# Kernel optimization log

Measured on AMD Instinct MI355X. Metric: run time of the kernel, lower is better.

Reference implementation:

```python
import jax, jax.numpy as jnp
import numpy as np

E = 1024
H = 16
D = E // H  # head_dim = 64


def setup_inputs() -> dict:
    key = jax.random.key(0)
    k_x, k_w1, k_b1, k_w2, k_b2 = jax.random.split(key, 5)
    s = 1.0 / np.sqrt(E)
    return {
        "x": jax.random.normal(k_x, (2, 2048, E), dtype=jnp.float32),
        "qkv_w": jax.random.uniform(k_w1, (3 * E, E), jnp.float32, -s, s),
        "qkv_b": jax.random.uniform(k_b1, (3 * E,), jnp.float32, -s, s),
        "out_w": jax.random.uniform(k_w2, (E, E), jnp.float32, -s, s),
        "out_b": jax.random.uniform(k_b2, (E,), jnp.float32, -s, s),
    }


def reference(x, qkv_w, qkv_b, out_w, out_b):
    B, T, _ = x.shape
    # qkv projection (torch Linear: x @ W.T + b)
    qkv = x @ qkv_w.T + qkv_b  # [B, T, 3E]
    q, k, v = jnp.split(qkv, 3, axis=-1)
    # [B, T, E] -> [B, H, T, D]
    def to_heads(t):
        return t.reshape(B, T, H, D).transpose(0, 2, 1, 3)
    q, k, v = to_heads(q), to_heads(k), to_heads(v)
    scale = 1.0 / np.sqrt(D).astype(np.float32)
    scores = jnp.einsum("bhqd,bhkd->bhqk", q, k) * scale  # [B, H, T, T]
    attn = jax.nn.softmax(scores, axis=-1)
    # dropout is identity in eval mode
    out = jnp.einsum("bhqk,bhkd->bhqd", attn, v)  # [B, H, T, D]
    out = out.transpose(0, 2, 1, 3).reshape(B, T, E)
    return out @ out_w.T + out_b
```

## Files before the change

kernel.cpp:

```cpp
#include <hip/hip_runtime.h>

#define TT 2048
#define BB 2
#define EE 1024
#define HH 16
#define DD 64
#define E3 3072
#define NTOK 4096

typedef unsigned short u16;
typedef _Float16 __attribute__((ext_vector_type(8))) half8;
typedef __fp16 __attribute__((ext_vector_type(2))) fp16x2;
typedef __attribute__((ext_vector_type(4))) float f32x4;

__device__ __forceinline__ unsigned f2h(float f) {
    union { _Float16 h; u16 u; } v; v.h = (_Float16)f; return (unsigned)v.u;
}
__device__ __forceinline__ unsigned pkh(float a, float b) {
    union { fp16x2 h; unsigned u; } v;
    v.h = __builtin_amdgcn_cvt_pkrtz(a, b);
    return v.u;
}

__device__ __forceinline__ void async_ld16(const u16* g, const u16* l) {
    auto gp = reinterpret_cast<const __attribute__((address_space(1))) unsigned*>(
        reinterpret_cast<uintptr_t>(g));
    auto lp = reinterpret_cast<__attribute__((address_space(3))) unsigned*>(
        reinterpret_cast<uintptr_t>(l));
    __builtin_amdgcn_global_load_lds(gp, lp, 16, 0, 0);
}

__global__ __launch_bounds__(256) void split3(
    const float* __restrict__ x, const float* __restrict__ w1,
    const float* __restrict__ w2,
    u16* __restrict__ xh, u16* __restrict__ w1h, u16* __restrict__ w2h)
{
    const int N1 = (NTOK * EE) / 4;
    const int N2 = N1 + (E3 * EE) / 4;
    int i = blockIdx.x * 256 + threadIdx.x;
    const float* src; u16* dst; int j;
    if (i < N1)      { src = x;  dst = xh;  j = i; }
    else if (i < N2) { src = w1; dst = w1h; j = i - N1; }
    else             { src = w2; dst = w2h; j = i - N2; }
    float4 v = ((const float4*)src)[j];
    *(uint2*)&dst[(size_t)j * 4] = make_uint2(
        f2h(v.x) | (f2h(v.y) << 16), f2h(v.z) | (f2h(v.w) << 16));
}

__global__ __launch_bounds__(256) void vtrans(
    const u16* __restrict__ qkv, u16* __restrict__ vt)
{
    __shared__ u16 L[64][72];
    const int tid = threadIdx.x;
    const int t0 = blockIdx.x * 64;
    const int h  = blockIdx.y;
    const int b  = blockIdx.z;
    const int row = tid >> 2;
    const int c16 = (tid & 3) << 4;

    const u16* src = qkv + (size_t)(b * TT + t0 + row) * E3 + 2 * EE + h * DD + c16;
    *(uint4*)&L[row][c16]     = *(const uint4*)src;
    *(uint4*)&L[row][c16 + 8] = *(const uint4*)(src + 8);
    __syncthreads();

    union { uint4 u[2]; u16 s[16]; } P;
#pragma unroll
    for (int j = 0; j < 16; ++j) P.s[j] = L[c16 + j][row];
    u16* dst = vt + ((size_t)(b * HH + h) * DD + row) * TT + t0 + c16;
    *(uint4*)dst       = P.u[0];
    *(uint4*)(dst + 8) = P.u[1];
}

template <int WMT, bool QSCALE, bool F16OUT>
__global__ __launch_bounds__(256, 3) void gemm_f16(
    const u16* __restrict__ Ag, const u16* __restrict__ Wg,
    const float* __restrict__ bias, void* __restrict__ Cout, int M, int N)
{
    constexpr int BM = WMT * 32;
    constexpr int APASS = BM / 32;
    __shared__ u16 sA[BM * 64];
    __shared__ u16 sB[128 * 64];

    const int tid  = threadIdx.x;
    const int lane = tid & 63;
    const int wave = tid >> 6;
    const int quad = lane >> 4;
    const int l16  = lane & 15;
    const int wm = wave >> 1, wn = wave & 1;
    const int m0 = blockIdx.y * BM;
    const int n0 = blockIdx.x * 128;

    const int srow = tid >> 3;
    const int schk = tid & 7;

    const u16* ag[APASS]; int aldw[APASS];
#pragma unroll
    for (int p = 0; p < APASS; ++p) {
        int row = p * 32 + srow;
        ag[p] = Ag + (size_t)(m0 + row) * EE + ((schk ^ (row & 7)) << 3);
        aldw[p] = (p * 256 + wave * 64) * 8;
    }
    const u16* bg[4]; int bldw[4];
#pragma unroll
    for (int p = 0; p < 4; ++p) {
        int row = p * 32 + srow;
        bg[p] = Wg + (size_t)(n0 + row) * EE + ((schk ^ (row & 7)) << 3);
        bldw[p] = (p * 256 + wave * 64) * 8;
    }

    f32x4 acc[WMT][4];
#pragma unroll
    for (int mt = 0; mt < WMT; ++mt)
#pragma unroll
        for (int nt = 0; nt < 4; ++nt) acc[mt][nt] = (f32x4){0.f, 0.f, 0.f, 0.f};

    for (int k0 = 0; k0 < EE; k0 += 64) {
        __syncthreads();
#pragma unroll
        for (int p = 0; p < APASS; ++p) async_ld16(ag[p] + k0, sA + aldw[p]);
#pragma unroll
        for (int p = 0; p < 4; ++p)    async_ld16(bg[p] + k0, sB + bldw[p]);
        __syncthreads();

        half8 fa[WMT][2], fb[4][2];
#pragma unroll
        for (int mt = 0; mt < WMT; ++mt) {
            int r = wm * (WMT * 16) + mt * 16 + l16;
#pragma unroll
            for (int ks = 0; ks < 2; ++ks)
                fa[mt][ks] = *(const half8*)&sA[r * 64 + (((ks * 4 + quad) ^ (r & 7)) << 3)];
        }
#pragma unroll
        for (int nt = 0; nt < 4; ++nt) {
            int r = wn * 64 + nt * 16 + l16;
#pragma unroll
            for (int ks = 0; ks < 2; ++ks)
                fb[nt][ks] = *(const half8*)&sB[r * 64 + (((ks * 4 + quad) ^ (r & 7)) << 3)];
        }
#pragma unroll
        for (int ks = 0; ks < 2; ++ks)
#pragma unroll
            for (int mt = 0; mt < WMT; ++mt)
#pragma unroll
                for (int nt = 0; nt < 4; ++nt)
                    acc[mt][nt] = __builtin_amdgcn_mfma_f32_16x16x32_f16(
                        fa[mt][ks], fb[nt][ks], acc[mt][nt], 0, 0, 0);
    }

    const float scale = (QSCALE && n0 < EE) ? 0.18033688011112042f : 1.0f;
    float bv[4];
#pragma unroll
    for (int nt = 0; nt < 4; ++nt) bv[nt] = bias[n0 + wn * 64 + nt * 16 + l16];
#pragma unroll
    for (int mt = 0; mt < WMT; ++mt)
#pragma unroll
        for (int nt = 0; nt < 4; ++nt)
#pragma unroll
            for (int r = 0; r < 4; ++r) {
                int rg = m0 + wm * (WMT * 16) + mt * 16 + quad * 4 + r;
                int cg = n0 + wn * 64 + nt * 16 + l16;
                float v = (acc[mt][nt][r] + bv[nt]) * scale;
                if (F16OUT) ((u16*)Cout)[(size_t)rg * N + cg] = (u16)f2h(v);
                else        ((float*)Cout)[(size_t)rg * N + cg] = v;
            }
}

__global__ __launch_bounds__(256, 3) void attn_mfma(
    const u16* __restrict__ qkv, const u16* __restrict__ vt,
    u16* __restrict__ obuf)
{
    __shared__ u16 KB[2][64][64];
    __shared__ u16 VB[2][64][64];
    __shared__ u16 QP[128][64];

    const int tid  = threadIdx.x;
    const int wave = tid >> 6;
    const int lane = tid & 63;
    const int quad = lane >> 4;
    const int l16  = lane & 15;

    const int q0 = blockIdx.x * 128;
    const int hh = blockIdx.y;
    const int b  = blockIdx.z;

    const int srow = tid >> 3;
    const int schk = tid & 7;
    const int ldsw = wave * 512;

#pragma unroll
    for (int p = 0; p < 4; ++p) {
        int row = p * 32 + srow;
        const u16* qg = qkv + (size_t)(b * TT + q0 + row) * E3 + hh * DD
                        + ((schk ^ (row & 7)) << 3);
        async_ld16(qg, &QP[0][0] + p * 2048 + ldsw);
    }
#pragma unroll
    for (int p = 0; p < 2; ++p) {
        int row = p * 32 + srow;
        int sw8 = (schk ^ (row & 7)) << 3;
        async_ld16(qkv + (size_t)(b * TT + row) * E3 + EE + hh * DD + sw8,
                   &KB[0][0][0] + p * 2048 + ldsw);
        async_ld16(vt + ((size_t)(b * HH + hh) * DD + row) * TT + sw8,
                   &VB[0][0][0] + p * 2048 + ldsw);
    }
    __syncthreads();

    half8 qb[2][2];
#pragma unroll
    for (int qt = 0; qt < 2; ++qt) {
        int row = wave * 32 + qt * 16 + l16;
#pragma unroll
        for (int ks = 0; ks < 2; ++ks)
            qb[qt][ks] = *(const half8*)&QP[row][((ks * 4 + quad) ^ (row & 7)) << 3];
    }

    const f32x4 Z = {0.f, 0.f, 0.f, 0.f};
    float l_i[2] = {0.f, 0.f};
    f32x4 o[4][2];
#pragma unroll
    for (int dt = 0; dt < 4; ++dt)
#pragma unroll
        for (int qt = 0; qt < 2; ++qt) o[dt][qt] = (f32x4){0.f, 0.f, 0.f, 0.f};

    int cur = 0;
    for (int kt = 0; kt < TT; kt += 64, cur ^= 1) {
        const int ktn = (kt + 64) & (TT - 1);
#pragma unroll
        for (int p = 0; p < 2; ++p) {
            int row = p * 32 + srow;
            int sw8 = (schk ^ (row & 7)) << 3;
            async_ld16(qkv + (size_t)(b * TT + ktn + row) * E3 + EE + hh * DD + sw8,
                       &KB[cur ^ 1][0][0] + p * 2048 + ldsw);
            async_ld16(vt + ((size_t)(b * HH + hh) * DD + row) * TT + ktn + sw8,
                       &VB[cur ^ 1][0][0] + p * 2048 + ldsw);
        }

        f32x4 s[2][4];
#pragma unroll
        for (int nt = 0; nt < 4; ++nt) {
            int r0 = nt * 16 + l16;
            half8 kf0 = *(const half8*)&KB[cur][r0][((quad)     ^ (r0 & 7)) << 3];
            half8 kf1 = *(const half8*)&KB[cur][r0][((4 + quad) ^ (r0 & 7)) << 3];
#pragma unroll
            for (int qt = 0; qt < 2; ++qt) {
                f32x4 t = __builtin_amdgcn_mfma_f32_16x16x32_f16(kf0, qb[qt][0], Z, 0, 0, 0);
                s[qt][nt] = __builtin_amdgcn_mfma_f32_16x16x32_f16(kf1, qb[qt][1], t, 0, 0, 0);
            }
        }

#pragma unroll
        for (int qt = 0; qt < 2; ++qt) {
            int prow = wave * 32 + qt * 16 + l16;
            float rs0 = 0.f, rs1 = 0.f;
#pragma unroll
            for (int nt = 0; nt < 4; ++nt) {
                float p0 = __builtin_amdgcn_exp2f(s[qt][nt][0]);
                float p1 = __builtin_amdgcn_exp2f(s[qt][nt][1]);
                float p2 = __builtin_amdgcn_exp2f(s[qt][nt][2]);
                float p3 = __builtin_amdgcn_exp2f(s[qt][nt][3]);
                rs0 += p0 + p1;
                rs1 += p2 + p3;
                int phys = (nt * 2 + (quad >> 1)) ^ (prow & 7);
                *(uint2*)&QP[prow][phys * 8 + ((quad & 1) << 2)] =
                    make_uint2(pkh(p0, p1), pkh(p2, p3));
            }
            l_i[qt] += rs0 + rs1;
        }

#pragma unroll
        for (int ks = 0; ks < 2; ++ks) {
            half8 pf[2];
#pragma unroll
            for (int qt = 0; qt < 2; ++qt) {
                int prow = wave * 32 + qt * 16 + l16;
                pf[qt] = *(const half8*)&QP[prow][((ks * 4 + quad) ^ (prow & 7)) << 3];
            }
#pragma unroll
            for (int dt = 0; dt < 4; ++dt) {
                int vr = dt * 16 + l16;
                half8 vf = *(const half8*)&VB[cur][vr][((ks * 4 + quad) ^ (vr & 7)) << 3];
#pragma unroll
                for (int qt = 0; qt < 2; ++qt)
                    o[dt][qt] = __builtin_amdgcn_mfma_f32_16x16x32_f16(vf, pf[qt], o[dt][qt], 0, 0, 0);
            }
        }

        __syncthreads();
    }

    float inv[2];
#pragma unroll
    for (int qt = 0; qt < 2; ++qt) {
        float l = l_i[qt];
        l += __shfl_xor(l, 16, 64);
        l += __shfl_xor(l, 32, 64);
        inv[qt] = 1.f / l;
    }
#pragma unroll
    for (int qt = 0; qt < 2; ++qt) {
        size_t base = (size_t)(b * TT + q0 + wave * 32 + qt * 16 + l16) * EE + hh * DD;
#pragma unroll
        for (int dt = 0; dt < 4; ++dt) {
            unsigned hv[4];
#pragma unroll
            for (int r = 0; r < 4; ++r) hv[r] = f2h(o[dt][qt][r] * inv[qt]);
            *(uint2*)&obuf[base + dt * 16 + quad * 4] =
                make_uint2(hv[0] | (hv[1] << 16), hv[2] | (hv[3] << 16));
        }
    }
}

extern "C" void kernel_launch(void* const* d_in, const int* in_sizes, int n_in,
                              void* d_out, int out_size, void* d_ws, size_t ws_size,
                              hipStream_t stream)
{
    const float* x     = (const float*)d_in[0];
    const float* qkv_w = (const float*)d_in[1];
    const float* qkv_b = (const float*)d_in[2];
    const float* out_w = (const float*)d_in[3];
    const float* out_b = (const float*)d_in[4];
    float* out = (float*)d_out;

    const size_t NX  = (size_t)NTOK * EE;
    const size_t NW1 = (size_t)E3 * EE;
    const size_t NW2 = (size_t)EE * EE;
    const size_t NQ  = (size_t)NTOK * E3;

    u16* ws   = (u16*)d_ws;
    u16* x_h  = ws;
    u16* w1h  = ws + NX;
    u16* w2h  = w1h + NW1;
    u16* qkvb = w2h + NW2;
    u16* vtb  = qkvb + NQ;

    split3<<<dim3((unsigned)((NX + NW1 + NW2) / 4 / 256)), 256, 0, stream>>>(
        x, qkv_w, out_w, x_h, w1h, w2h);

    gemm_f16<4, true, true><<<dim3(E3 / 128, NTOK / 128), 256, 0, stream>>>(
        x_h, w1h, qkv_b, (void*)qkvb, NTOK, E3);

    vtrans<<<dim3(TT / 64, HH, BB), 256, 0, stream>>>(qkvb, vtb);

    attn_mfma<<<dim3(TT / 128, HH, BB), 256, 0, stream>>>(qkvb, vtb, x_h);

    gemm_f16<2, false, false><<<dim3(EE / 128, NTOK / 64), 256, 0, stream>>>(
        x_h, w2h, out_b, (void*)out, NTOK, EE);
}
```

Baseline: 189.4 us.

## Load K and V fragments directly from global into registers, dropping LDS staging

The attention kernel no longer stages K and V tiles through double-buffered shared memory with async copies and a per-iteration block barrier. Each wave now loads its MFMA K and V fragments straight from global memory into registers, prefetching the next K tile into a ping-pong register set across a two-step unrolled loop. Launch bounds drop from 3 to 2 blocks per SM to make room for the extra registers. The cost is that the four waves of a block each fetch the same K/V data (more cache traffic, uncoalesced row-strided loads) and occupancy is lower.

Result: slower. 261.2 us (+37.9%).

```diff
diff --git a/kernel.cpp b/kernel.cpp
--- a/kernel.cpp
+++ b/kernel.cpp
@@ -165,12 +165,10 @@
             }
 }
 
-__global__ __launch_bounds__(256, 3) void attn_mfma(
+__global__ __launch_bounds__(256, 2) void attn_mfma(
     const u16* __restrict__ qkv, const u16* __restrict__ vt,
     u16* __restrict__ obuf)
 {
-    __shared__ u16 KB[2][64][64];
-    __shared__ u16 VB[2][64][64];
     __shared__ u16 QP[128][64];
 
     const int tid  = threadIdx.x;
@@ -183,36 +181,18 @@
     const int hh = blockIdx.y;
     const int b  = blockIdx.z;
 
-    const int srow = tid >> 3;
-    const int schk = tid & 7;
-    const int ldsw = wave * 512;
-
-#pragma unroll
-    for (int p = 0; p < 4; ++p) {
-        int row = p * 32 + srow;
-        const u16* qg = qkv + (size_t)(b * TT + q0 + row) * E3 + hh * DD
-                        + ((schk ^ (row & 7)) << 3);
-        async_ld16(qg, &QP[0][0] + p * 2048 + ldsw);
-    }
-#pragma unroll
-    for (int p = 0; p < 2; ++p) {
-        int row = p * 32 + srow;
-        int sw8 = (schk ^ (row & 7)) << 3;
-        async_ld16(qkv + (size_t)(b * TT + row) * E3 + EE + hh * DD + sw8,
-                   &KB[0][0][0] + p * 2048 + ldsw);
-        async_ld16(vt + ((size_t)(b * HH + hh) * DD + row) * TT + sw8,
-                   &VB[0][0][0] + p * 2048 + ldsw);
-    }
-    __syncthreads();
-
     half8 qb[2][2];
 #pragma unroll
     for (int qt = 0; qt < 2; ++qt) {
-        int row = wave * 32 + qt * 16 + l16;
+        const u16* qg = qkv + (size_t)(b * TT + q0 + wave * 32 + qt * 16 + l16) * E3
+                        + hh * DD + quad * 8;
 #pragma unroll
         for (int ks = 0; ks < 2; ++ks)
-            qb[qt][ks] = *(const half8*)&QP[row][((ks * 4 + quad) ^ (row & 7)) << 3];
-    }
+            qb[qt][ks] = *(const half8*)(qg + ks * 32);
+    }
+
+    const u16* kbase = qkv + (size_t)(b * TT) * E3 + EE + hh * DD + quad * 8;
+    const u16* vbase = vt + (size_t)(b * HH + hh) * DD * TT + quad * 8;
 
     const f32x4 Z = {0.f, 0.f, 0.f, 0.f};
     float l_i[2] = {0.f, 0.f};
@@ -222,31 +202,39 @@
 #pragma unroll
         for (int qt = 0; qt < 2; ++qt) o[dt][qt] = (f32x4){0.f, 0.f, 0.f, 0.f};
 
-    int cur = 0;
-    for (int kt = 0; kt < TT; kt += 64, cur ^= 1) {
-        const int ktn = (kt + 64) & (TT - 1);
-#pragma unroll
-        for (int p = 0; p < 2; ++p) {
-            int row = p * 32 + srow;
-            int sw8 = (schk ^ (row & 7)) << 3;
-            async_ld16(qkv + (size_t)(b * TT + ktn + row) * E3 + EE + hh * DD + sw8,
-                       &KB[cur ^ 1][0][0] + p * 2048 + ldsw);
-            async_ld16(vt + ((size_t)(b * HH + hh) * DD + row) * TT + ktn + sw8,
-                       &VB[cur ^ 1][0][0] + p * 2048 + ldsw);
-        }
+    half8 ka[8], kb2[8];
+#pragma unroll
+    for (int nt = 0; nt < 4; ++nt)
+#pragma unroll
+        for (int ks = 0; ks < 2; ++ks)
+            ka[nt * 2 + ks] =
+                *(const half8*)(kbase + (size_t)(nt * 16 + l16) * E3 + ks * 32);
+
+    auto subiter = [&](int ktc, int ktn, half8* kcur, half8* knx) {
+        half8 vf[8];
+#pragma unroll
+        for (int dt = 0; dt < 4; ++dt)
+#pragma unroll
+            for (int ks = 0; ks < 2; ++ks)
+                vf[dt * 2 + ks] = *(const half8*)
+                    (vbase + (size_t)(dt * 16 + l16) * TT + ktc + ks * 32);
+#pragma unroll
+        for (int nt = 0; nt < 4; ++nt)
+#pragma unroll
+            for (int ks = 0; ks < 2; ++ks)
+                knx[nt * 2 + ks] = *(const half8*)
+                    (kbase + (size_t)(ktn + nt * 16 + l16) * E3 + ks * 32);
 
         f32x4 s[2][4];
 #pragma unroll
-        for (int nt = 0; nt < 4; ++nt) {
-            int r0 = nt * 16 + l16;
-            half8 kf0 = *(const half8*)&KB[cur][r0][((quad)     ^ (r0 & 7)) << 3];
-            half8 kf1 = *(const half8*)&KB[cur][r0][((4 + quad) ^ (r0 & 7)) << 3];
+        for (int nt = 0; nt < 4; ++nt)
 #pragma unroll
             for (int qt = 0; qt < 2; ++qt) {
-                f32x4 t = __builtin_amdgcn_mfma_f32_16x16x32_f16(kf0, qb[qt][0], Z, 0, 0, 0);
-                s[qt][nt] = __builtin_amdgcn_mfma_f32_16x16x32_f16(kf1, qb[qt][1], t, 0, 0, 0);
+                f32x4 t = __builtin_amdgcn_mfma_f32_16x16x32_f16(
+                    kcur[nt * 2 + 0], qb[qt][0], Z, 0, 0, 0);
+                s[qt][nt] = __builtin_amdgcn_mfma_f32_16x16x32_f16(
+                    kcur[nt * 2 + 1], qb[qt][1], t, 0, 0, 0);
             }
-        }
 
 #pragma unroll
         for (int qt = 0; qt < 2; ++qt) {
@@ -276,16 +264,17 @@
                 pf[qt] = *(const half8*)&QP[prow][((ks * 4 + quad) ^ (prow & 7)) << 3];
             }
 #pragma unroll
-            for (int dt = 0; dt < 4; ++dt) {
-                int vr = dt * 16 + l16;
-                half8 vf = *(const half8*)&VB[cur][vr][((ks * 4 + quad) ^ (vr & 7)) << 3];
+            for (int dt = 0; dt < 4; ++dt)
 #pragma unroll
                 for (int qt = 0; qt < 2; ++qt)
-                    o[dt][qt] = __builtin_amdgcn_mfma_f32_16x16x32_f16(vf, pf[qt], o[dt][qt], 0, 0, 0);
-            }
-        }
-
-        __syncthreads();
+                    o[dt][qt] = __builtin_amdgcn_mfma_f32_16x16x32_f16(
+                        vf[dt * 2 + ks], pf[qt], o[dt][qt], 0, 0, 0);
+        }
+    };
+
+    for (int kt = 0; kt < TT; kt += 128) {
+        subiter(kt,      kt + 64,              ka,  kb2);
+        subiter(kt + 64, (kt + 128) & (TT - 1), kb2, ka);
     }
 
     float inv[2];
```
